# Kernel tuning notes

Measured on AMD Instinct MI355X. Metric: run time of the kernel, lower is better.

Reference implementation:

```python
import jax, jax.numpy as jnp
import numpy as np

N = 50000          # nodes
E = 1600000        # edges (avg degree 32)
G = 256            # graphs in batch
IN_DIM = 128
HID = 64
NUM_LAYERS = 12    # stacked layers after the first
NUM_REL = 3
NEG_SLOPE = 0.2    # RGATConv default leaky_relu slope


def setup_inputs() -> dict:
    key = jax.random.key(0)
    ks = jax.random.split(key, 12)
    return {
        "node_features": jax.random.normal(ks[0], (N, IN_DIM), jnp.float32),
        "edge_index": jax.random.randint(ks[1], (2, E), 0, N, jnp.int32),
        "edge_type": jax.random.randint(ks[2], (E,), 0, NUM_REL, jnp.int32),
        "batch_index": jnp.sort(jax.random.randint(ks[3], (N,), 0, G, jnp.int32)),
        "W_first": jax.random.normal(ks[4], (NUM_REL, IN_DIM, HID), jnp.float32) / np.sqrt(IN_DIM).astype(np.float32),
        "q_first": jax.random.normal(ks[5], (HID,), jnp.float32) / np.sqrt(HID).astype(np.float32),
        "k_first": jax.random.normal(ks[6], (HID,), jnp.float32) / np.sqrt(HID).astype(np.float32),
        "b_first": jnp.zeros((HID,), jnp.float32),
        "W_stack": jax.random.normal(ks[7], (NUM_LAYERS, NUM_REL, HID, HID), jnp.float32) / np.sqrt(HID).astype(np.float32),
        "q_stack": jax.random.normal(ks[8], (NUM_LAYERS, HID), jnp.float32) / np.sqrt(HID).astype(np.float32),
        "k_stack": jax.random.normal(ks[9], (NUM_LAYERS, HID), jnp.float32) / np.sqrt(HID).astype(np.float32),
        "b_stack": jnp.zeros((NUM_LAYERS, HID), jnp.float32),
        "t": jnp.ones((1,), jnp.float32),
    }


def _segment_softmax(logits, seg, num_segments):
    # numerically-stable softmax over entries sharing a segment id (PyG `softmax`)
    m = jax.ops.segment_max(logits, seg, num_segments=num_segments)
    m = jnp.where(jnp.isfinite(m), m, 0.0)  # empty segments -> -inf, neutralize
    e = jnp.exp(logits - m[seg])
    s = jax.ops.segment_sum(e, seg, num_segments=num_segments)
    return e / (s[seg] + 1e-16)


def _rgat_layer(x, W, q, k, b, src, dst, etype):
    # PyG RGATConv, heads=1, dim=1, additive-self-attention, across-relation softmax.
    n = x.shape[0]
    xr = jnp.einsum('ni,rio->rno', x, W)       # [R,N,H] per-relation transform of all nodes
    qn = jnp.einsum('rno,o->rn', xr, q)        # [R,N] query scalar (out_i @ q)
    kn = jnp.einsum('rno,o->rn', xr, k)        # [R,N] key scalar   (out_j @ k)
    logits = jax.nn.leaky_relu(qn[etype, dst] + kn[etype, src], NEG_SLOPE)  # [E]
    alpha = _segment_softmax(logits, dst, n)   # softmax over incoming edges of each dst
    msg = alpha[:, None] * xr[etype, src]      # [E,H]
    return jax.ops.segment_sum(msg, dst, num_segments=n) + b


def reference(node_features, edge_index, edge_type, batch_index,
              W_first, q_first, k_first, b_first,
              W_stack, q_stack, k_stack, b_stack, t):
    src, dst = edge_index[0], edge_index[1]   # PyG convention: row=source j, col=target i
    x1 = _rgat_layer(node_features, W_first, q_first, k_first, b_first, src, dst, edge_type)

    def step(x, p):
        W, q, k, b = p
        y = _rgat_layer(x, W, q, k, b, src, dst, edge_type)
        return y, y

    _, ys = jax.lax.scan(step, x1, (W_stack, q_stack, k_stack, b_stack))
    all_x = jnp.concatenate([x1[None], ys], axis=0)                 # [13,N,H]
    node_rep = jnp.transpose(all_x, (1, 0, 2)).reshape(node_features.shape[0], -1)  # [N,13*H]

    # SoftmaxAggregation(learn=True): per-feature softmax over nodes of each graph
    alpha_g = _segment_softmax(node_rep * t[0], batch_index, G)     # [N,13*H]
    graph_rep = jax.ops.segment_sum(node_rep * alpha_g, batch_index, num_segments=G)
    return graph_rep, node_rep
```

## Files before the change

### kernel.cpp

```cpp
#include <hip/hip_runtime.h>
#include <math.h>

#define NN 50000
#define NE 1600000
#define NG 256
#define IND 128
#define HID 64
#define NREL 3
#define SLOPE 0.2f
#define XRS 192
#define NRS 832
#define WTP 136

typedef short bf16x8 __attribute__((ext_vector_type(8)));
typedef float f32x4 __attribute__((ext_vector_type(4)));

__device__ __forceinline__ float wred_max(float v){
  #pragma unroll
  for (int o = 32; o; o >>= 1) v = fmaxf(v, __shfl_xor(v, o));
  return v;
}
__device__ __forceinline__ float wred_sum(float v){
  #pragma unroll
  for (int o = 32; o; o >>= 1) v += __shfl_xor(v, o);
  return v;
}

__device__ __forceinline__ unsigned short f2bf(float f){
  unsigned int u = __float_as_uint(f);
  u = (u + 0x7FFFu + ((u >> 16) & 1u)) >> 16;
  return (unsigned short)u;
}
__device__ __forceinline__ float bf2f(unsigned short h){
  return __uint_as_float(((unsigned int)h) << 16);
}


__global__ void hist_kernel(const int* __restrict__ dst, int* __restrict__ cnts){
  int e = blockIdx.x * blockDim.x + threadIdx.x;
  if (e < NE) atomicAdd(&cnts[dst[e]], 1);
}

__global__ void scan1_kernel(const int* __restrict__ cnts, int* __restrict__ rowp,
                             int* __restrict__ bsum){
  __shared__ int ws[16];
  int b = blockIdx.x, tid = threadIdx.x;
  int i = b * 1024 + tid;
  int lane = tid & 63, wid = tid >> 6;
  int v = (i < NN) ? cnts[i] : 0;
  int x = v;
  #pragma unroll
  for (int o = 1; o < 64; o <<= 1){ int t = __shfl_up(x, o); if (lane >= o) x += t; }
  if (lane == 63) ws[wid] = x;
  __syncthreads();
  if (tid < 16){
    int y = ws[tid];
    #pragma unroll
    for (int o = 1; o < 16; o <<= 1){ int t = __shfl_up(y, o); if (tid >= o) y += t; }
    ws[tid] = y;
  }
  __syncthreads();
  int off = (wid > 0) ? ws[wid - 1] : 0;
  x += off;
  if (i < NN) rowp[i] = x - v;
  if (tid == 1023) bsum[b] = x;
}

__global__ void scan2_kernel(int* __restrict__ bsum, int* __restrict__ rowp, int nb){
  int tid = threadIdx.x;
  int v = (tid < nb) ? bsum[tid] : 0;
  int x = v;
  #pragma unroll
  for (int o = 1; o < 64; o <<= 1){ int t = __shfl_up(x, o); if (tid >= o) x += t; }
  if (tid < nb) bsum[tid] = x - v;
  if (tid == 63) rowp[NN] = x;
}

__global__ void scan3_kernel(int* __restrict__ rowp, const int* __restrict__ bsum){
  int i = blockIdx.x * 1024 + threadIdx.x;
  if (i < NN) rowp[i] += bsum[blockIdx.x];
}

__global__ void scatter_kernel(const int* __restrict__ src, const int* __restrict__ dst,
                               const int* __restrict__ et, const int* __restrict__ rowp,
                               int* __restrict__ fill, int* __restrict__ csr){
  int e = blockIdx.x * blockDim.x + threadIdx.x;
  if (e >= NE) return;
  int d = dst[e];
  int pos = atomicAdd(&fill[d], 1);
  csr[rowp[d] + pos] = src[e] | (et[e] << 24);
}

__global__ void gstart_kernel(const int* __restrict__ batch, int* __restrict__ gst){
  int n = blockIdx.x * blockDim.x + threadIdx.x;
  if (n > NN) return;
  int bc = (n < NN) ? batch[n] : NG;
  int bp = (n == 0) ? -1 : batch[n - 1];
  for (int g = bp + 1; g <= bc; ++g) gst[g] = n;
}

__global__ void wprep_kernel(const float* __restrict__ W, unsigned short* __restrict__ Wtg, int K){
  int i = blockIdx.x * blockDim.x + threadIdx.x;
  if (i >= NREL * K * HID) return;
  int h = i & 63;
  int k = (i >> 6) % K;
  int r = i / (K * HID);
  Wtg[(size_t)((r << 6) + h) * K + k] = f2bf(W[i]);
}

__global__ __launch_bounds__(256) void mm_kernel(
    const float* __restrict__ x, int ldx, int K,
    const unsigned short* __restrict__ Wtg,
    const float* __restrict__ qv, const float* __restrict__ kv,
    unsigned short* __restrict__ XRb, float* __restrict__ QK){
  __shared__ unsigned short Wt[192 * WTP];
  int tid = threadIdx.x;
  int w = tid >> 6, lane = tid & 63;
  int lrow = lane & 15, kg = lane >> 4;
  int row0 = blockIdx.x * 64;
  int row = row0 + w * 16 + lrow;
  int nb8 = 192 * (K >> 3);
  for (int i = tid; i < nb8; i += 256){
    int col = i / (K >> 3);
    int k8 = (i - col * (K >> 3)) << 3;
    *(bf16x8*)&Wt[col * WTP + k8] = *(const bf16x8*)&Wtg[(size_t)col * K + k8];
  }
  __syncthreads();

  f32x4 acc[12];
  #pragma unroll
  for (int t = 0; t < 12; ++t) acc[t] = (f32x4){0.f, 0.f, 0.f, 0.f};

  int ksteps = K >> 5;
  for (int ks = 0; ks < ksteps; ++ks){
    bf16x8 xb;
    if (row < NN){
      const float* xp = x + (size_t)row * ldx + (ks << 5) + (kg << 3);
      float4 v0 = *(const float4*)xp;
      float4 v1 = *(const float4*)(xp + 4);
      xb[0] = (short)f2bf(v0.x); xb[1] = (short)f2bf(v0.y);
      xb[2] = (short)f2bf(v0.z); xb[3] = (short)f2bf(v0.w);
      xb[4] = (short)f2bf(v1.x); xb[5] = (short)f2bf(v1.y);
      xb[6] = (short)f2bf(v1.z); xb[7] = (short)f2bf(v1.w);
    } else {
      #pragma unroll
      for (int j = 0; j < 8; ++j) xb[j] = 0;
    }
    int kk = (ks << 5) + (kg << 3);
    #pragma unroll
    for (int t = 0; t < 12; ++t){
      bf16x8 wf = *(const bf16x8*)&Wt[(t * 16 + lrow) * WTP + kk];
      acc[t] = __builtin_amdgcn_mfma_f32_16x16x32_bf16(wf, xb, acc[t], 0, 0, 0);
    }
  }

  if (row < NN){
    unsigned short* orow = XRb + (size_t)row * XRS;
    #pragma unroll
    for (int t = 0; t < 12; ++t){
      ushort4 o4;
      o4.x = f2bf(acc[t][0]); o4.y = f2bf(acc[t][1]);
      o4.z = f2bf(acc[t][2]); o4.w = f2bf(acc[t][3]);
      *(ushort4*)(orow + t * 16 + (kg << 2)) = o4;
    }
  }

  float pq[3] = {0,0,0}, pk[3] = {0,0,0};
  #pragma unroll
  for (int t = 0; t < 12; ++t){
    int r = t >> 2;
    int hbase = ((t & 3) << 4) + (kg << 2);
    #pragma unroll
    for (int j = 0; j < 4; ++j){
      float qc = qv[hbase + j], kc = kv[hbase + j];
      pq[r] = fmaf(acc[t][j], qc, pq[r]);
      pk[r] = fmaf(acc[t][j], kc, pk[r]);
    }
  }
  #pragma unroll
  for (int o = 16; o < 64; o <<= 1){
    #pragma unroll
    for (int r = 0; r < 3; ++r){
      pq[r] += __shfl_xor(pq[r], o);
      pk[r] += __shfl_xor(pk[r], o);
    }
  }
  if (kg == 0 && row < NN){
    #pragma unroll
    for (int r = 0; r < 3; ++r){
      QK[row * 8 + r] = pq[r];
      QK[row * 8 + 3 + r] = pk[r];
    }
  }
}


__global__ __launch_bounds__(256) void edge_kernel(
    const unsigned short* __restrict__ XRb, const float* __restrict__ QK,
    const int* __restrict__ csr, const int* __restrict__ rowp,
    const float* __restrict__ bias, float* __restrict__ out){
  int wid = blockIdx.x * 4 + (threadIdx.x >> 6);
  int lane = threadIdx.x & 63;
  if (wid >= NN) return;
  int beg = rowp[wid], end = rowp[wid + 1];
  int cnt = end - beg;
  float* orow = out + (size_t)wid * NRS;
  int sub = lane & 7;
  int g   = lane >> 3;
  if (cnt == 0){
    if (lane < 8){
      float4 b0 = *(const float4*)(bias + sub * 8);
      float4 b1 = *(const float4*)(bias + sub * 8 + 4);
      *(float4*)(orow + sub * 8) = b0;
      *(float4*)(orow + sub * 8 + 4) = b1;
    }
    return;
  }
  float q0 = QK[wid * 8], q1 = QK[wid * 8 + 1], q2 = QK[wid * 8 + 2];

  if (cnt <= 128){
    float l0 = -INFINITY, l1 = -INFINITY;
    int o0 = 0, o1 = 0;
    {
      int idx = beg + lane;
      if (idx < end){
        int pk = csr[idx];
        int sn = pk & 0xFFFFFF, et = pk >> 24;
        float lg = (et == 0 ? q0 : (et == 1 ? q1 : q2)) + QK[sn * 8 + 3 + et];
        l0 = lg >= 0.f ? lg : lg * SLOPE;
        o0 = sn * XRS + et * HID;
      }
      idx += 64;
      if (idx < end){
        int pk = csr[idx];
        int sn = pk & 0xFFFFFF, et = pk >> 24;
        float lg = (et == 0 ? q0 : (et == 1 ? q1 : q2)) + QK[sn * 8 + 3 + et];
        l1 = lg >= 0.f ? lg : lg * SLOPE;
        o1 = sn * XRS + et * HID;
      }
    }
    float m = wred_max(fmaxf(l0, l1));
    float e0 = __expf(l0 - m), e1 = __expf(l1 - m);
    float s = wred_sum(e0 + e1);
    float inv = 1.f / (s + 1e-16f);
    float w0 = e0 * inv, w1 = e1 * inv;

    const unsigned short* xp = XRb + sub * 8;
    float acc[8] = {};
    int nA = min(cnt, 64);
    #pragma unroll 2
    for (int e = 0; e < nA; e += 8){
      int sl = e + g;
      float we = __shfl(w0, sl);
      int   oe = __shfl(o0, sl);
      uint4 d = *(const uint4*)(xp + oe);
      acc[0] = fmaf(we, __uint_as_float(d.x << 16), acc[0]);
      acc[1] = fmaf(we, __uint_as_float(d.x & 0xFFFF0000u), acc[1]);
      acc[2] = fmaf(we, __uint_as_float(d.y << 16), acc[2]);
      acc[3] = fmaf(we, __uint_as_float(d.y & 0xFFFF0000u), acc[3]);
      acc[4] = fmaf(we, __uint_as_float(d.z << 16), acc[4]);
      acc[5] = fmaf(we, __uint_as_float(d.z & 0xFFFF0000u), acc[5]);
      acc[6] = fmaf(we, __uint_as_float(d.w << 16), acc[6]);
      acc[7] = fmaf(we, __uint_as_float(d.w & 0xFFFF0000u), acc[7]);
    }
    if (cnt > 64){
      int nB = cnt - 64;
      #pragma unroll 2
      for (int e = 0; e < nB; e += 8){
        int sl = e + g;
        float we = __shfl(w1, sl);
        int   oe = __shfl(o1, sl);
        uint4 d = *(const uint4*)(xp + oe);
        acc[0] = fmaf(we, __uint_as_float(d.x << 16), acc[0]);
        acc[1] = fmaf(we, __uint_as_float(d.x & 0xFFFF0000u), acc[1]);
        acc[2] = fmaf(we, __uint_as_float(d.y << 16), acc[2]);
        acc[3] = fmaf(we, __uint_as_float(d.y & 0xFFFF0000u), acc[3]);
        acc[4] = fmaf(we, __uint_as_float(d.z << 16), acc[4]);
        acc[5] = fmaf(we, __uint_as_float(d.z & 0xFFFF0000u), acc[5]);
        acc[6] = fmaf(we, __uint_as_float(d.w << 16), acc[6]);
        acc[7] = fmaf(we, __uint_as_float(d.w & 0xFFFF0000u), acc[7]);
      }
    }
    #pragma unroll
    for (int o = 8; o < 64; o <<= 1)
      #pragma unroll
      for (int j = 0; j < 8; ++j)
        acc[j] += __shfl_xor(acc[j], o);
    if (lane < 8){
      float4 b0 = *(const float4*)(bias + sub * 8);
      float4 b1 = *(const float4*)(bias + sub * 8 + 4);
      float4 r0, r1;
      r0.x = acc[0] + b0.x; r0.y = acc[1] + b0.y; r0.z = acc[2] + b0.z; r0.w = acc[3] + b0.w;
      r1.x = acc[4] + b1.x; r1.y = acc[5] + b1.y; r1.z = acc[6] + b1.z; r1.w = acc[7] + b1.w;
      *(float4*)(orow + sub * 8) = r0;
      *(float4*)(orow + sub * 8 + 4) = r1;
    }
    return;
  }

  float bv = bias[lane];
  float m = -INFINITY, s = 0.f;
  for (int c = beg; c < end; c += 64){
    int idx = c + lane;
    float l = -INFINITY;
    if (idx < end){
      int pk = csr[idx];
      int sn = pk & 0xFFFFFF, et = pk >> 24;
      float lg = (et == 0 ? q0 : (et == 1 ? q1 : q2)) + QK[sn * 8 + 3 + et];
      l = lg >= 0.f ? lg : lg * SLOPE;
    }
    float mnew = fmaxf(m, wred_max(l));
    float ps = wred_sum((idx < end) ? __expf(l - mnew) : 0.f);
    s = s * __expf(m - mnew) + ps;
    m = mnew;
  }
  float inv = 1.f / (s + 1e-16f);
  float acc = 0.f;
  for (int c = beg; c < end; c += 64){
    int idx = c + lane;
    int off = 0; float wgt = 0.f;
    if (idx < end){
      int pk = csr[idx];
      int sn = pk & 0xFFFFFF, et = pk >> 24;
      float lg = (et == 0 ? q0 : (et == 1 ? q1 : q2)) + QK[sn * 8 + 3 + et];
      float l = lg >= 0.f ? lg : lg * SLOPE;
      wgt = __expf(l - m) * inv;
      off = sn * XRS + et * HID;
    }
    int cc = min(64, end - c);
    #pragma unroll 4
    for (int j = 0; j < cc; ++j){
      float wj = __uint_as_float(__builtin_amdgcn_readlane(__float_as_uint(wgt), j));
      int oj = __builtin_amdgcn_readlane(off, j);
      acc = fmaf(wj, bf2f(XRb[oj + lane]), acc);
    }
  }
  orow[lane] = acc + bv;
}


__global__ __launch_bounds__(256) void agg_kernel(
    const float* __restrict__ nr, const int* __restrict__ gst,
    const float* __restrict__ tp, float* __restrict__ out){
  __shared__ float red[4][64];
  __shared__ float red2[4][64];
  int g = blockIdx.x;
  int lane = threadIdx.x & 63;
  int w = threadIdx.x >> 6;
  int f = blockIdx.y * 64 + lane;
  int s = gst[g], e = gst[g + 1];
  float tval = tp[0];
  float m = -INFINITY;
  for (int n = s + w; n < e; n += 4)
    m = fmaxf(m, nr[(size_t)n * NRS + f] * tval);
  red[w][lane] = m;
  __syncthreads();
  m = fmaxf(fmaxf(red[0][lane], red[1][lane]), fmaxf(red[2][lane], red[3][lane]));
  float ss = 0.f, acc = 0.f;
  for (int n = s + w; n < e; n += 4){
    float v = nr[(size_t)n * NRS + f];
    float ee = __expf(v * tval - m);
    ss += ee; acc = fmaf(v, ee, acc);
  }
  __syncthreads();
  red[w][lane] = ss; red2[w][lane] = acc;
  __syncthreads();
  if (w == 0){
    ss = red[0][lane] + red[1][lane] + red[2][lane] + red[3][lane];
    acc = red2[0][lane] + red2[1][lane] + red2[2][lane] + red2[3][lane];
    out[(size_t)g * NRS + f] = acc / (ss + 1e-16f);
  }
}


extern "C" void kernel_launch(void* const* d_in, const int* in_sizes, int n_in,
                              void* d_out, int out_size, void* d_ws, size_t ws_size,
                              hipStream_t stream){
  const float* x0   = (const float*)d_in[0];
  const int*   eidx = (const int*)d_in[1];
  const int*   etyp = (const int*)d_in[2];
  const int*   batch= (const int*)d_in[3];
  const float* Wf   = (const float*)d_in[4];
  const float* qf   = (const float*)d_in[5];
  const float* kf   = (const float*)d_in[6];
  const float* bf   = (const float*)d_in[7];
  const float* Ws   = (const float*)d_in[8];
  const float* qs   = (const float*)d_in[9];
  const float* ks   = (const float*)d_in[10];
  const float* bs   = (const float*)d_in[11];
  const float* tp   = (const float*)d_in[12];

  float* gout = (float*)d_out;
  float* nrep = gout + (size_t)NG * NRS;

  char* w = (char*)d_ws;
  unsigned short* XRb = (unsigned short*)w; w += (size_t)NN * XRS * 2;
  float* QK   = (float*)w;  w += (size_t)NN * 8 * 4;
  unsigned short* Wtg = (unsigned short*)w; w += (size_t)192 * IND * 2;
  int*   rowp = (int*)w;    w += (size_t)(NN + 2) * 4;
  int*   cnts = (int*)w;    w += (size_t)NN * 4;
  int*   gst  = (int*)w;    w += (size_t)(NG + 2) * 4;
  int*   bsum = (int*)w;    w += 64 * 4;
  int*   csr  = (int*)w;    w += (size_t)NE * 4;

  const int* srcv = eidx;
  const int* dstv = eidx + NE;

  const int NB = (NN + 1023) / 1024;

  hipMemsetAsync(cnts, 0, (size_t)NN * 4, stream);
  hist_kernel<<<(NE + 255) / 256, 256, 0, stream>>>(dstv, cnts);
  scan1_kernel<<<NB, 1024, 0, stream>>>(cnts, rowp, bsum);
  scan2_kernel<<<1, 64, 0, stream>>>(bsum, rowp, NB);
  scan3_kernel<<<NB, 1024, 0, stream>>>(rowp, bsum);
  hipMemsetAsync(cnts, 0, (size_t)NN * 4, stream);
  scatter_kernel<<<(NE + 255) / 256, 256, 0, stream>>>(srcv, dstv, etyp, rowp, cnts, csr);
  gstart_kernel<<<(NN + 256) / 256, 256, 0, stream>>>(batch, gst);

  for (int l = 0; l < 13; ++l){
    int K = (l == 0) ? IND : HID;
    const float* W  = (l == 0) ? Wf : (Ws + (size_t)(l - 1) * NREL * HID * HID);
    const float* q  = (l == 0) ? qf : (qs + (size_t)(l - 1) * HID);
    const float* kv = (l == 0) ? kf : (ks + (size_t)(l - 1) * HID);
    const float* b  = (l == 0) ? bf : (bs + (size_t)(l - 1) * HID);
    const float* x  = (l == 0) ? x0 : (nrep + (size_t)(l - 1) * HID);
    int ldx = (l == 0) ? IND : NRS;
    int tot = NREL * K * HID;
    wprep_kernel<<<(tot + 255) / 256, 256, 0, stream>>>(W, Wtg, K);
    mm_kernel<<<(NN + 63) / 64, 256, 0, stream>>>(x, ldx, K, Wtg, q, kv, XRb, QK);
    edge_kernel<<<(NN + 3) / 4, 256, 0, stream>>>(XRb, QK, csr, rowp, b, nrep + (size_t)l * HID);
  }
  dim3 ag(NG, 13);
  agg_kernel<<<ag, 256, 0, stream>>>(nrep, gst, tp, gout);
}
```

Before: 1.053 ms.

## Batch weight prep into one launch, prefetch edge gather operands, online-softmax aggregation

Converts all 13 layers' weights to bf16 transposed layout in a single upfront kernel instead of one small launch per layer, removing 12 launches from the serial chain. In the edge kernel, the shuffled weights and offsets for up to 8 edge groups are gathered first and the loads are fully unrolled with early break, so more independent memory loads can be in flight. The graph aggregation switches to a single-pass online softmax, reading node_rep once instead of twice, at the cost of extra exps per element.

After: 1.016 ms. 1.04x faster.

```diff
diff --git a/kernel.cpp b/kernel.cpp
--- a/kernel.cpp
+++ b/kernel.cpp
@@ -11,6 +11,9 @@
 #define XRS 192
 #define NRS 832
 #define WTP 136
+#define W0SZ (192*128)
+#define WLSZ (192*64)
+#define WTOT (W0SZ + 12*WLSZ)
 
 typedef short bf16x8 __attribute__((ext_vector_type(8)));
 typedef float f32x4 __attribute__((ext_vector_type(4)));
@@ -99,13 +102,23 @@
   for (int g = bp + 1; g <= bc; ++g) gst[g] = n;
 }
 
-__global__ void wprep_kernel(const float* __restrict__ W, unsigned short* __restrict__ Wtg, int K){
+__global__ void wprep13_kernel(const float* __restrict__ Wf, const float* __restrict__ Ws,
+                               unsigned short* __restrict__ Wtg13){
   int i = blockIdx.x * blockDim.x + threadIdx.x;
-  if (i >= NREL * K * HID) return;
-  int h = i & 63;
-  int k = (i >> 6) % K;
-  int r = i / (K * HID);
-  Wtg[(size_t)((r << 6) + h) * K + k] = f2bf(W[i]);
+  if (i >= WTOT) return;
+  int j, K; size_t base; const float* W;
+  if (i < W0SZ){ j = i; K = IND; base = 0; W = Wf; }
+  else {
+    int t = i - W0SZ;
+    int l = t / WLSZ;
+    j = t - l * WLSZ; K = HID;
+    base = W0SZ + (size_t)l * WLSZ;
+    W = Ws + (size_t)l * WLSZ;
+  }
+  int h = j & 63;
+  int k = (j >> 6) % K;
+  int r = j / (K * HID);
+  Wtg13[base + (size_t)((r << 6) + h) * K + k] = f2bf(W[j]);
 }
 
 __global__ __launch_bounds__(256) void mm_kernel(
@@ -247,13 +260,19 @@
 
     const unsigned short* xp = XRb + sub * 8;
     float acc[8] = {};
-    int nA = min(cnt, 64);
-    #pragma unroll 2
-    for (int e = 0; e < nA; e += 8){
-      int sl = e + g;
-      float we = __shfl(w0, sl);
-      int   oe = __shfl(o0, sl);
-      uint4 d = *(const uint4*)(xp + oe);
+
+    float wS[8]; int oS[8];
+    #pragma unroll
+    for (int e = 0; e < 8; ++e){
+      int sl = (e << 3) + g;
+      wS[e] = __shfl(w0, sl);
+      oS[e] = __shfl(o0, sl);
+    }
+    int nIt = (min(cnt, 64) + 7) >> 3;
+    #pragma unroll
+    for (int e = 0; e < 8; ++e){
+      uint4 d = *(const uint4*)(xp + oS[e]);
+      float we = wS[e];
       acc[0] = fmaf(we, __uint_as_float(d.x << 16), acc[0]);
       acc[1] = fmaf(we, __uint_as_float(d.x & 0xFFFF0000u), acc[1]);
       acc[2] = fmaf(we, __uint_as_float(d.y << 16), acc[2]);
@@ -262,15 +281,20 @@
       acc[5] = fmaf(we, __uint_as_float(d.z & 0xFFFF0000u), acc[5]);
       acc[6] = fmaf(we, __uint_as_float(d.w << 16), acc[6]);
       acc[7] = fmaf(we, __uint_as_float(d.w & 0xFFFF0000u), acc[7]);
+      if (e + 1 >= nIt) break;
     }
     if (cnt > 64){
-      int nB = cnt - 64;
-      #pragma unroll 2
-      for (int e = 0; e < nB; e += 8){
-        int sl = e + g;
-        float we = __shfl(w1, sl);
-        int   oe = __shfl(o1, sl);
-        uint4 d = *(const uint4*)(xp + oe);
+      #pragma unroll
+      for (int e = 0; e < 8; ++e){
+        int sl = (e << 3) + g;
+        wS[e] = __shfl(w1, sl);
+        oS[e] = __shfl(o1, sl);
+      }
+      int nIt2 = (cnt - 64 + 7) >> 3;
+      #pragma unroll
+      for (int e = 0; e < 8; ++e){
+        uint4 d = *(const uint4*)(xp + oS[e]);
+        float we = wS[e];
         acc[0] = fmaf(we, __uint_as_float(d.x << 16), acc[0]);
         acc[1] = fmaf(we, __uint_as_float(d.x & 0xFFFF0000u), acc[1]);
         acc[2] = fmaf(we, __uint_as_float(d.y << 16), acc[2]);
@@ -279,6 +303,7 @@
         acc[5] = fmaf(we, __uint_as_float(d.z & 0xFFFF0000u), acc[5]);
         acc[6] = fmaf(we, __uint_as_float(d.w << 16), acc[6]);
         acc[7] = fmaf(we, __uint_as_float(d.w & 0xFFFF0000u), acc[7]);
+        if (e + 1 >= nIt2) break;
       }
     }
     #pragma unroll
@@ -342,33 +367,37 @@
 __global__ __launch_bounds__(256) void agg_kernel(
     const float* __restrict__ nr, const int* __restrict__ gst,
     const float* __restrict__ tp, float* __restrict__ out){
-  __shared__ float red[4][64];
-  __shared__ float red2[4][64];
+  __shared__ float rm[4][64], rs[4][64], ra[4][64];
   int g = blockIdx.x;
   int lane = threadIdx.x & 63;
   int w = threadIdx.x >> 6;
   int f = blockIdx.y * 64 + lane;
   int s = gst[g], e = gst[g + 1];
   float tval = tp[0];
-  float m = -INFINITY;
-  for (int n = s + w; n < e; n += 4)
-    m = fmaxf(m, nr[(size_t)n * NRS + f] * tval);
-  red[w][lane] = m;
-  __syncthreads();
-  m = fmaxf(fmaxf(red[0][lane], red[1][lane]), fmaxf(red[2][lane], red[3][lane]));
-  float ss = 0.f, acc = 0.f;
+  float m = -INFINITY, ss = 0.f, ac = 0.f;
   for (int n = s + w; n < e; n += 4){
     float v = nr[(size_t)n * NRS + f];
-    float ee = __expf(v * tval - m);
-    ss += ee; acc = fmaf(v, ee, acc);
-  }
-  __syncthreads();
-  red[w][lane] = ss; red2[w][lane] = acc;
+    float vm = v * tval;
+    float Mn = fmaxf(m, vm);
+    float sc = __expf(m - Mn);
+    float ev = __expf(vm - Mn);
+    ss = ss * sc + ev;
+    ac = ac * sc + v * ev;
+    m = Mn;
+  }
+  rm[w][lane] = m; rs[w][lane] = ss; ra[w][lane] = ac;
   __syncthreads();
   if (w == 0){
-    ss = red[0][lane] + red[1][lane] + red[2][lane] + red[3][lane];
-    acc = red2[0][lane] + red2[1][lane] + red2[2][lane] + red2[3][lane];
-    out[(size_t)g * NRS + f] = acc / (ss + 1e-16f);
+    float M = fmaxf(fmaxf(rm[0][lane], rm[1][lane]), fmaxf(rm[2][lane], rm[3][lane]));
+    float S = 0.f, A = 0.f;
+    #pragma unroll
+    for (int i = 0; i < 4; ++i){
+      float si = rs[i][lane];
+      float sci = (si > 0.f) ? __expf(rm[i][lane] - M) : 0.f;
+      S = fmaf(si, sci, S);
+      A = fmaf(ra[i][lane], sci, A);
+    }
+    out[(size_t)g * NRS + f] = A / (S + 1e-16f);
   }
 }
 
@@ -396,7 +425,7 @@
   char* w = (char*)d_ws;
   unsigned short* XRb = (unsigned short*)w; w += (size_t)NN * XRS * 2;
   float* QK   = (float*)w;  w += (size_t)NN * 8 * 4;
-  unsigned short* Wtg = (unsigned short*)w; w += (size_t)192 * IND * 2;
+  unsigned short* Wtg13 = (unsigned short*)w; w += (size_t)WTOT * 2;
   int*   rowp = (int*)w;    w += (size_t)(NN + 2) * 4;
   int*   cnts = (int*)w;    w += (size_t)NN * 4;
   int*   gst  = (int*)w;    w += (size_t)(NG + 2) * 4;
@@ -416,17 +445,16 @@
   hipMemsetAsync(cnts, 0, (size_t)NN * 4, stream);
   scatter_kernel<<<(NE + 255) / 256, 256, 0, stream>>>(srcv, dstv, etyp, rowp, cnts, csr);
   gstart_kernel<<<(NN + 256) / 256, 256, 0, stream>>>(batch, gst);
+  wprep13_kernel<<<(WTOT + 255) / 256, 256, 0, stream>>>(Wf, Ws, Wtg13);
 
   for (int l = 0; l < 13; ++l){
     int K = (l == 0) ? IND : HID;
-    const float* W  = (l == 0) ? Wf : (Ws + (size_t)(l - 1) * NREL * HID * HID);
+    const unsigned short* Wtg = Wtg13 + ((l == 0) ? 0 : (W0SZ + (size_t)(l - 1) * WLSZ));
     const float* q  = (l == 0) ? qf : (qs + (size_t)(l - 1) * HID);
     const float* kv = (l == 0) ? kf : (ks + (size_t)(l - 1) * HID);
     const float* b  = (l == 0) ? bf : (bs + (size_t)(l - 1) * HID);
     const float* x  = (l == 0) ? x0 : (nrep + (size_t)(l - 1) * HID);
     int ldx = (l == 0) ? IND : NRS;
-    int tot = NREL * K * HID;
-    wprep_kernel<<<(tot + 255) / 256, 256, 0, stream>>>(W, Wtg, K);
     mm_kernel<<<(NN + 63) / 64, 256, 0, stream>>>(x, ldx, K, Wtg, q, kv, XRb, QK);
     edge_kernel<<<(NN + 3) / 4, 256, 0, stream>>>(XRb, QK, csr, rowp, b, nrep + (size_t)l * HID);
   }
```
